# Performance work log

Hardware: AMD Instinct MI355X
Metric: run time of the kernel (lower is better)

Reference implementation:

```python
import jax, jax.numpy as jnp
import numpy as np

V, E, H = 32000, 512, 1024
S_LEN, T_LEN = 2048, 2048


def setup_inputs() -> dict:
    key = jax.random.key(0)
    ks = jax.random.split(key, 16)
    u = lambda k, shape: jax.random.uniform(k, shape, jnp.float32, -0.1, 0.1)
    return {
        "source": jax.random.randint(ks[0], (1, S_LEN), 0, V),
        "target": jax.random.randint(ks[1], (1, T_LEN), 0, V),
        "emb": u(ks[2], (V, E)),
        "enc_Wih": u(ks[3], (H, E)),
        "enc_bih": u(ks[4], (H,)),
        "enc_Whh": u(ks[5], (H, H)),
        "enc_bhh": u(ks[6], (H,)),
        "dec_Wih": u(ks[7], (H, E)),
        "dec_bih": u(ks[8], (H,)),
        "dec_Whh": u(ks[9], (H, H)),
        "dec_bhh": u(ks[10], (H,)),
        "proj_W": u(ks[11], (H, 2 * H)),
        "proj_b": u(ks[12], (H,)),
        "out_W": u(ks[13], (V, H)),
        "out_b": u(ks[14], (V,)),
    }


def _run_rnn(Wih, bih, Whh, bhh, x, h0):
    # x: [B, T, E]; vanilla RNN: h_t = tanh(x_t Wih^T + bih + h_{t-1} Whh^T + bhh)
    def step(h, xt):
        hn = jnp.tanh(xt @ Wih.T + bih + h @ Whh.T + bhh)
        return hn, hn
    h_last, ys = jax.lax.scan(step, h0, jnp.swapaxes(x, 0, 1))  # ys: [T, B, H]
    return jnp.swapaxes(ys, 0, 1), h_last


def reference(source, target, emb, enc_Wih, enc_bih, enc_Whh, enc_bhh,
              dec_Wih, dec_bih, dec_Whh, dec_bhh, proj_W, proj_b, out_W, out_b):
    B = source.shape[0]
    h0 = jnp.zeros((B, H), dtype=emb.dtype)

    src_emb = emb[source]                                        # [B, S, E]
    enc_out, h = _run_rnn(enc_Wih, enc_bih, enc_Whh, enc_bhh, src_emb, h0)
    tgt_emb = emb[target]                                        # [B, T, E]
    dec_out, _ = _run_rnn(dec_Wih, dec_bih, dec_Whh, dec_bhh, tgt_emb, h)

    # attention: target queries over source encodings
    aff = jnp.einsum('bth,bsh->bts', dec_out, enc_out)           # [B, T, S]
    attn = jax.nn.softmax(aff, axis=-1)
    ctx = jnp.einsum('bts,bsh->bth', attn, enc_out)              # [B, T, H]

    proj = jnp.concatenate([dec_out, ctx], axis=-1) @ proj_W.T + proj_b  # [B, T, H]
    scores = proj @ out_W.T + out_b                              # [B, T, V]

    logits = scores[:, :-1].reshape(-1, V)                       # [B*(T-1), V]
    tgt = target[:, 1:].reshape(-1)
    logp = jax.nn.log_softmax(logits, axis=-1)
    loss = -jnp.sum(jnp.take_along_axis(logp, tgt[:, None], axis=1))
    return loss
```

## Files before the change

### kernel.cpp

```cpp
#include <hip/hip_runtime.h>
#include <math.h>

typedef unsigned short u16;
typedef unsigned int   u32;

#define V_SZ   32000
#define E_SZ   512
#define H_SZ   1024
#define S_LEN  2048
#define T_LEN  2048
#define G_RNN  64
#define RPW    16
#define NTILE_V (V_SZ / 128)

typedef __attribute__((ext_vector_type(8))) short bf16x8;
typedef __attribute__((ext_vector_type(4))) float f32x4;
typedef __attribute__((ext_vector_type(4))) unsigned int u32x4;

typedef __attribute__((address_space(3))) void* lds_vp;
typedef const __attribute__((address_space(1))) void* gbl_vp;

__device__ __forceinline__ float bf2f(u16 u) { return __uint_as_float(((u32)u) << 16); }
__device__ __forceinline__ u16 f2bf(float f) {
  u32 x = __float_as_uint(f);
  return (u16)((x + 0x7fffu + ((x >> 16) & 1u)) >> 16);
}
__device__ __forceinline__ bool f32_bad(float f) {
  return (__float_as_uint(f) & 0x7F800000u) == 0x7F800000u;
}
__device__ __forceinline__ bool bf_bad(u16 u) { return (u & 0x7F80u) == 0x7F80u; }

__device__ __forceinline__ bf16x8 cvt8(float4 a, float4 b) {
  bf16x8 r;
  r[0] = (short)f2bf(a.x); r[1] = (short)f2bf(a.y);
  r[2] = (short)f2bf(a.z); r[3] = (short)f2bf(a.w);
  r[4] = (short)f2bf(b.x); r[5] = (short)f2bf(b.y);
  r[6] = (short)f2bf(b.z); r[7] = (short)f2bf(b.w);
  return r;
}

__global__ void sentinel_kernel(float* out) { out[0] = -400.0f; }
__global__ void diag_kernel(float* out, float code) { out[0] = code; }

__global__ __launch_bounds__(256) void init_kernel(
    const float* __restrict__ enc_bih, const float* __restrict__ enc_bhh,
    const float* __restrict__ dec_bih, const float* __restrict__ dec_bhh,
    float* biasE, float* biasD,
    u32* hsync, float* loss_acc, float* prog)
{
  int i = blockIdx.x * blockDim.x + threadIdx.x;
  if (i < H_SZ) {
    biasE[i] = enc_bih[i] + enc_bhh[i];
    biasD[i] = dec_bih[i] + dec_bhh[i];
  }
  if (i < 2 * H_SZ)
    __hip_atomic_store(hsync + i, 0u, __ATOMIC_RELAXED, __HIP_MEMORY_SCOPE_AGENT);
  if (i == 0)    { loss_acc[0] = 0.f; prog[0] = 1.0f; }
  if (i >= 1 && i < 16) prog[i] = 0.f;
}

__global__ __launch_bounds__(256) void gather_kernel(
    const float* __restrict__ emb, const int* __restrict__ ids, u16* __restrict__ dst,
    float* prog, int pidx)
{
  const int row = blockIdx.x;
  const int id  = ids[row];
  const float2* s = (const float2*)(emb + (size_t)id * E_SZ);
  const float2 v = s[threadIdx.x];
  const u32 pack = (u32)f2bf(v.x) | ((u32)f2bf(v.y) << 16);
  ((u32*)(dst + (size_t)row * E_SZ))[threadIdx.x] = pack;
  if (row == 0 && threadIdx.x == 0) prog[pidx] = 1.0f;
}

template<int MODE, int BF32>
__global__ __launch_bounds__(256) void gemm_bt(
    const u16* __restrict__ A, int lda,
    const void* __restrict__ Bp, int ldb,
    const float* __restrict__ bias,
    u16* __restrict__ Cbf, int ldc,
    float* __restrict__ stats, int ntiles, int K,
    float* prog, int pidx)
{
  __shared__ __align__(16) u16 As[128 * 32];
  __shared__ __align__(16) u16 Bs[128 * 32];
  __shared__ float sst[2][128][2];

  const int tid  = threadIdx.x;
  const int wave = tid >> 6;
  const int lane = tid & 63;
  const int quad = lane >> 4;
  const int l16  = lane & 15;
  const int m0 = blockIdx.y * 128;
  const int n0 = blockIdx.x * 128;
  const int wm = (wave >> 1) * 64;
  const int wn = (wave & 1) * 64;

  f32x4 acc[4][4];
#pragma unroll
  for (int i = 0; i < 4; ++i)
#pragma unroll
    for (int j = 0; j < 4; ++j) acc[i][j] = (f32x4){0.f, 0.f, 0.f, 0.f};

  const int srow = lane >> 2;
  const int scol = (lane & 3) * 8;
  const int c0   = wave * 2;
  const u16* ga0 = A + (size_t)(m0 + (c0 + 0) * 16 + srow) * lda + scol;
  const u16* ga1 = A + (size_t)(m0 + (c0 + 1) * 16 + srow) * lda + scol;
  const u16*   B16 = (const u16*)Bp;
  const float* B32 = (const float*)Bp;
  const u16* gb0 = B16 + (size_t)(n0 + (c0 + 0) * 16 + srow) * ldb + scol;
  const u16* gb1 = B16 + (size_t)(n0 + (c0 + 1) * 16 + srow) * ldb + scol;
  const float* fb0 = B32 + (size_t)(n0 + (c0 + 0) * 16 + srow) * ldb + scol;
  const float* fb1 = B32 + (size_t)(n0 + (c0 + 1) * 16 + srow) * ldb + scol;

  for (int k0 = 0; k0 < K; k0 += 32) {
    __builtin_amdgcn_global_load_lds((gbl_vp)(ga0 + k0), (lds_vp)(&As[(c0 + 0) * 512]), 16, 0, 0);
    __builtin_amdgcn_global_load_lds((gbl_vp)(ga1 + k0), (lds_vp)(&As[(c0 + 1) * 512]), 16, 0, 0);
    if (BF32) {
      const float* p0 = fb0 + k0;
      const float* p1 = fb1 + k0;
      const float4 a0 = *(const float4*)p0, a1 = *(const float4*)(p0 + 4);
      const float4 b0 = *(const float4*)p1, b1 = *(const float4*)(p1 + 4);
      *(bf16x8*)&Bs[(c0 + 0) * 512 + lane * 8] = cvt8(a0, a1);
      *(bf16x8*)&Bs[(c0 + 1) * 512 + lane * 8] = cvt8(b0, b1);
    } else {
      __builtin_amdgcn_global_load_lds((gbl_vp)(gb0 + k0), (lds_vp)(&Bs[(c0 + 0) * 512]), 16, 0, 0);
      __builtin_amdgcn_global_load_lds((gbl_vp)(gb1 + k0), (lds_vp)(&Bs[(c0 + 1) * 512]), 16, 0, 0);
    }
    __syncthreads();

    bf16x8 af[4], bg[4];
#pragma unroll
    for (int i = 0; i < 4; ++i) {
      af[i] = *(const bf16x8*)&As[(wm + i * 16 + l16) * 32 + quad * 8];
      bg[i] = *(const bf16x8*)&Bs[(wn + i * 16 + l16) * 32 + quad * 8];
    }
#pragma unroll
    for (int mi = 0; mi < 4; ++mi)
#pragma unroll
      for (int ni = 0; ni < 4; ++ni)
        acc[mi][ni] = __builtin_amdgcn_mfma_f32_16x16x32_bf16(af[mi], bg[ni], acc[mi][ni], 0, 0, 0);
    __syncthreads();
  }

  if (MODE == 2) {
#pragma unroll
    for (int mi = 0; mi < 4; ++mi) {
#pragma unroll
      for (int rr = 0; rr < 4; ++rr) {
        float v[4];
        float vmax = -1e30f;
#pragma unroll
        for (int ni = 0; ni < 4; ++ni) {
          const int col = n0 + wn + ni * 16 + l16;
          v[ni] = acc[mi][ni][rr] + (bias ? bias[col] : 0.f);
          vmax = fmaxf(vmax, v[ni]);
        }
        for (int d = 1; d < 16; d <<= 1) vmax = fmaxf(vmax, __shfl_xor(vmax, d, 64));
        float vs = 0.f;
#pragma unroll
        for (int ni = 0; ni < 4; ++ni) vs += expf(v[ni] - vmax);
        for (int d = 1; d < 16; d <<= 1) vs += __shfl_xor(vs, d, 64);
        if (l16 == 0) {
          const int lr = wm + mi * 16 + quad * 4 + rr;
          sst[wave & 1][lr][0] = vmax;
          sst[wave & 1][lr][1] = vs;
        }
      }
    }
    __syncthreads();
    if (tid < 128) {
      const float ma = sst[0][tid][0], sa = sst[0][tid][1];
      const float mb = sst[1][tid][0], sb = sst[1][tid][1];
      const float M = fmaxf(ma, mb);
      const float S = sa * expf(ma - M) + sb * expf(mb - M);
      const size_t row = (size_t)(m0 + tid);
      stats[(row * ntiles + blockIdx.x) * 2 + 0] = M;
      stats[(row * ntiles + blockIdx.x) * 2 + 1] = S;
    }
  } else {
#pragma unroll
    for (int mi = 0; mi < 4; ++mi)
#pragma unroll
      for (int ni = 0; ni < 4; ++ni) {
        const int col = n0 + wn + ni * 16 + l16;
        const float bb = bias ? bias[col] : 0.f;
#pragma unroll
        for (int rr = 0; rr < 4; ++rr) {
          const int row = m0 + wm + mi * 16 + quad * 4 + rr;
          Cbf[(size_t)row * ldc + col] = f2bf(acc[mi][ni][rr] + bb);
        }
      }
  }
  if (prog && blockIdx.x == 0 && blockIdx.y == 0 && tid == 0) prog[pidx] = 1.0f;
}

__global__ __launch_bounds__(256) void rnn_kernel(
    const float* __restrict__ Whh, const u16* __restrict__ pre,
    u16* __restrict__ hist, int ldh, const u16* __restrict__ h0,
    u16* __restrict__ outT,
    u32* __restrict__ hsync, int tagbase, int T, float* prog, int pidx)
{
  __shared__ float part[2][4][RPW];

  const int tid  = threadIdx.x;
  const int wg   = blockIdx.x;
  const int wv   = tid >> 6;
  const int lane = tid & 63;
  const int pr4  = tid << 2;

  float wreg[RPW][4];
#pragma unroll
  for (int r = 0; r < RPW; ++r) {
    const float4 v = *(const float4*)(Whh + (size_t)(wg * RPW + r) * H_SZ + pr4);
    wreg[r][0] = v.x; wreg[r][1] = v.y; wreg[r][2] = v.z; wreg[r][3] = v.w;
  }

  for (int t = 0; t < T; ++t) {
    float pv = 0.f;
    if (tid < RPW) pv = bf2f(pre[(size_t)t * H_SZ + wg * RPW + tid]);

    float h0v, h1v, h2v, h3v;
    if (t == 0) {
      if (h0) {
        const ushort4 hv = *(const ushort4*)(h0 + pr4);
        h0v = bf2f(hv.x); h1v = bf2f(hv.y); h2v = bf2f(hv.z); h3v = bf2f(hv.w);
      } else { h0v = h1v = h2v = h3v = 0.f; }
    } else {
      const u32 want = (u32)(tagbase + t);
      const u32* hs = hsync + (((t - 1) & 1) << 10) + pr4;
      u32 w0, w1, w2, w3;
      u32 spin = 0;
      for (;;) {
        if ((spin++ & 15u) == 15u) {
          w0 = __hip_atomic_load(hs + 0, __ATOMIC_RELAXED, __HIP_MEMORY_SCOPE_AGENT);
          w1 = __hip_atomic_load(hs + 1, __ATOMIC_RELAXED, __HIP_MEMORY_SCOPE_AGENT);
          w2 = __hip_atomic_load(hs + 2, __ATOMIC_RELAXED, __HIP_MEMORY_SCOPE_AGENT);
          w3 = __hip_atomic_load(hs + 3, __ATOMIC_RELAXED, __HIP_MEMORY_SCOPE_AGENT);
        } else {
          u32x4 x;
          asm volatile("global_load_dwordx4 %0, %1, off sc0 sc1\n\t"
                       "s_waitcnt vmcnt(0)"
                       : "=v"(x) : "v"(hs) : "memory");
          w0 = x[0]; w1 = x[1]; w2 = x[2]; w3 = x[3];
        }
        if ((w0 >> 16) == want && (w1 >> 16) == want &&
            (w2 >> 16) == want && (w3 >> 16) == want) break;
      }
      h0v = bf2f((u16)w0); h1v = bf2f((u16)w1);
      h2v = bf2f((u16)w2); h3v = bf2f((u16)w3);
    }

    float p[RPW];
#pragma unroll
    for (int r = 0; r < RPW; ++r)
      p[r] = wreg[r][0] * h0v + wreg[r][1] * h1v
           + wreg[r][2] * h2v + wreg[r][3] * h3v;

#pragma unroll
    for (int i = 0; i < 8; ++i) {
      const float send = (lane & 32) ? p[i] : p[i + 8];
      const float recv = __shfl_xor(send, 32, 64);
      const float keep = (lane & 32) ? p[i + 8] : p[i];
      p[i] = keep + recv;
    }
#pragma unroll
    for (int i = 0; i < 4; ++i) {
      const float send = (lane & 16) ? p[i] : p[i + 4];
      const float recv = __shfl_xor(send, 16, 64);
      const float keep = (lane & 16) ? p[i + 4] : p[i];
      p[i] = keep + recv;
    }
#pragma unroll
    for (int i = 0; i < 2; ++i) {
      const float send = (lane & 8) ? p[i] : p[i + 2];
      const float recv = __shfl_xor(send, 8, 64);
      const float keep = (lane & 8) ? p[i + 2] : p[i];
      p[i] = keep + recv;
    }
    {
      const float send = (lane & 4) ? p[0] : p[1];
      const float recv = __shfl_xor(send, 4, 64);
      const float keep = (lane & 4) ? p[1] : p[0];
      p[0] = keep + recv;
    }
    p[0] += __shfl_xor(p[0], 1, 64);
    p[0] += __shfl_xor(p[0], 2, 64);

    const int rown = (lane >> 2) & 15;
    if ((lane & 3) == 0) part[t & 1][wv][rown] = p[0];
    __syncthreads();

    if (tid < RPW) {
      const float s = part[t & 1][0][tid] + part[t & 1][1][tid]
                    + part[t & 1][2][tid] + part[t & 1][3][tid];
      const float hn = tanhf(pv + s);
      const u16 hv16 = f2bf(hn);
      const int gr = wg * RPW + tid;
      const u32 word = ((u32)(tagbase + t + 1) << 16) | (u32)hv16;
      __hip_atomic_store(hsync + ((t & 1) << 10) + gr, word,
                         __ATOMIC_RELAXED, __HIP_MEMORY_SCOPE_AGENT);
      hist[(size_t)t * ldh + gr] = hv16;
      if (outT) outT[(size_t)gr * S_LEN + t] = hv16;
    }
  }
  if (wg == 0 && tid == 0) prog[pidx] = 1.0f;
}

__global__ __launch_bounds__(256) void softmax_kernel(
    u16* __restrict__ aff, float* prog, int pidx)
{
  const int row = blockIdx.x;
  const int tid = threadIdx.x;
  u16* a = aff + (size_t)row * S_LEN;
  __shared__ float red[256];

  float m = -1e30f;
  for (int j = tid; j < S_LEN; j += 256) m = fmaxf(m, bf2f(a[j]));
  red[tid] = m; __syncthreads();
  for (int s = 128; s > 0; s >>= 1) { if (tid < s) red[tid] = fmaxf(red[tid], red[tid + s]); __syncthreads(); }
  const float M = red[0];
  __syncthreads();

  float sum = 0.f;
  for (int j = tid; j < S_LEN; j += 256) sum += expf(bf2f(a[j]) - M);
  red[tid] = sum; __syncthreads();
  for (int s = 128; s > 0; s >>= 1) { if (tid < s) red[tid] += red[tid + s]; __syncthreads(); }
  const float inv = 1.f / red[0];

  for (int j = tid; j < S_LEN; j += 256) {
    const float e = expf(bf2f(a[j]) - M) * inv;
    a[j] = f2bf(e);
  }
  if (row == 0 && tid == 0) prog[pidx] = 1.0f;
}

__global__ __launch_bounds__(256) void loss_kernel(
    const u16* __restrict__ proj_bf, const float* __restrict__ outW,
    const float* __restrict__ outb, const int* __restrict__ target,
    const float* __restrict__ stats, int ntiles, float* loss_acc,
    float* prog, int pidx)
{
  const int t   = blockIdx.x;
  const int tid = threadIdx.x;
  const int c   = target[t + 1];
  __shared__ float s1[256], s2[256];

  float p = 0.f;
  const u16*   pr = proj_bf + (size_t)t * H_SZ;
  const float* wr = outW + (size_t)c * H_SZ;
  for (int j = tid; j < H_SZ; j += 256) p += bf2f(pr[j]) * f2bf(wr[j]) * 0.f + bf2f(pr[j]) * bf2f(f2bf(wr[j]));
  s1[tid] = p; __syncthreads();
  for (int s = 128; s > 0; s >>= 1) { if (tid < s) s1[tid] += s1[tid + s]; __syncthreads(); }
  const float dotv = s1[0] + outb[c];

  const float* st = stats + (size_t)t * ntiles * 2;
  float mi = -1e30f, si = 0.f;
  if (tid < ntiles) { mi = st[tid * 2]; si = st[tid * 2 + 1]; }
  s2[tid] = mi; __syncthreads();
  for (int s = 128; s > 0; s >>= 1) { if (tid < s) s2[tid] = fmaxf(s2[tid], s2[tid + s]); __syncthreads(); }
  const float M = s2[0];
  const float e = (tid < ntiles) ? si * expf(mi - M) : 0.f;
  __syncthreads();
  s1[tid] = e; __syncthreads();
  for (int s = 128; s > 0; s >>= 1) { if (tid < s) s1[tid] += s1[tid + s]; __syncthreads(); }

  if (tid == 0) {
    atomicAdd(loss_acc, (M + logf(s1[0])) - dotv);
    if (t == 0) prog[pidx] = 1.0f;
  }
}

__global__ void finalize_kernel(
    const float* loss_acc, const float* prog,
    const float* biasE, const float* biasD,
    const u16* enc_out, const u16* cat, const u16* proj_bf, const float* stats,
    float* out)
{
  for (int i = 0; i < 13; ++i)
    if (prog[i] != 1.0f) { out[0] = -(100.0f + i); return; }

  const float loss = loss_acc[0];
  if (!f32_bad(loss)) { out[0] = loss; return; }

  int s = -1;
  for (int i = 0; i < 37 && s < 0; ++i)
    if (f32_bad(biasE[(i * 97) % H_SZ]) || f32_bad(biasD[(i * 97) % H_SZ])) s = 0;
  for (int i = 0; i < 37 && s < 0; ++i)
    if (bf_bad(enc_out[((size_t)i * 131071u) % (2048u * 1024u)])) s = 2;
  for (int i = 0; i < 37 && s < 0; ++i)
    if (bf_bad(cat[(((size_t)(i * 557) % 2048) * 2048) + (i * 97) % 1024])) s = 3;
  for (int i = 0; i < 37 && s < 0; ++i)
    if (bf_bad(cat[(((size_t)(i * 557) % 2048) * 2048) + 1024 + (i * 97) % 1024])) s = 5;
  for (int i = 0; i < 37 && s < 0; ++i)
    if (bf_bad(proj_bf[((size_t)i * 131071u) % (2048u * 1024u)])) s = 6;
  for (int i = 0; i < 37 && s < 0; ++i)
    if (f32_bad(stats[((size_t)i * 99991u) % (2048u * 500u)])) s = 7;
  out[0] = (s < 0) ? -300.0f : -(200.0f + 10.0f * s);
}

extern "C" void kernel_launch(void* const* d_in, const int* in_sizes, int n_in,
                              void* d_out, int out_size, void* d_ws, size_t ws_size,
                              hipStream_t stream)
{
  (void)in_sizes; (void)n_in; (void)out_size;

  const int*   src     = (const int*)d_in[0];
  const int*   tgt     = (const int*)d_in[1];
  const float* emb     = (const float*)d_in[2];
  const float* enc_Wih = (const float*)d_in[3];
  const float* enc_bih = (const float*)d_in[4];
  const float* enc_Whh = (const float*)d_in[5];
  const float* enc_bhh = (const float*)d_in[6];
  const float* dec_Wih = (const float*)d_in[7];
  const float* dec_bih = (const float*)d_in[8];
  const float* dec_Whh = (const float*)d_in[9];
  const float* dec_bhh = (const float*)d_in[10];
  const float* proj_W  = (const float*)d_in[11];
  const float* proj_b  = (const float*)d_in[12];
  const float* out_W   = (const float*)d_in[13];
  const float* out_b   = (const float*)d_in[14];

  char* wsb = (char*)d_ws;
  const size_t MB = (size_t)1 << 20;
  u16*   src_emb  = (u16*)(wsb + 0);
  u16*   tgt_emb  = (u16*)(wsb + 2 * MB);
  u16*   enc_outT = (u16*)(wsb + 0);
  u16*   proj_bf  = (u16*)(wsb + 0);
  u16*   enc_pre  = (u16*)(wsb + 4 * MB);
  u16*   dec_pre  = (u16*)(wsb + 8 * MB);
  u16*   aff      = (u16*)(wsb + 4 * MB);
  float* stats    = (float*)(wsb + 4 * MB);
  u16*   enc_out  = (u16*)(wsb + 12 * MB);
  u16*   cat      = (u16*)(wsb + 16 * MB);
  char*  tail     = wsb + 24 * MB;
  float* biasE    = (float*)tail;
  float* biasD    = biasE + H_SZ;
  float* loss_acc = biasD + H_SZ;
  float* prog     = loss_acc + 64;
  u32*   hsync    = (u32*)(prog + 64);
  const size_t need = 24 * MB + 64 * 1024;

  if (ws_size < need) {
    diag_kernel<<<1, 1, 0, stream>>>((float*)d_out, -(1000.0f + (float)(ws_size / MB)));
    return;
  }

  sentinel_kernel<<<1, 1, 0, stream>>>((float*)d_out);

  init_kernel<<<S_LEN / 256, 256, 0, stream>>>(enc_bih, enc_bhh, dec_bih, dec_bhh,
      biasE, biasD, hsync, loss_acc, prog);

  gather_kernel<<<S_LEN, 256, 0, stream>>>(emb, src, src_emb, prog, 1);
  gather_kernel<<<T_LEN, 256, 0, stream>>>(emb, tgt, tgt_emb, prog, 2);

  gemm_bt<1, 1><<<dim3(H_SZ / 128, S_LEN / 128), 256, 0, stream>>>(
      src_emb, E_SZ, enc_Wih, E_SZ, biasE, enc_pre, H_SZ, nullptr, 0, E_SZ, prog, 3);
  gemm_bt<1, 1><<<dim3(H_SZ / 128, T_LEN / 128), 256, 0, stream>>>(
      tgt_emb, E_SZ, dec_Wih, E_SZ, biasD, dec_pre, H_SZ, nullptr, 0, E_SZ, prog, 4);

  rnn_kernel<<<G_RNN, 256, 0, stream>>>(enc_Whh, enc_pre, enc_out, H_SZ, nullptr,
      enc_outT, hsync, 0, S_LEN, prog, 5);
  rnn_kernel<<<G_RNN, 256, 0, stream>>>(dec_Whh, dec_pre, cat, 2 * H_SZ,
      enc_out + (size_t)(S_LEN - 1) * H_SZ, nullptr, hsync, S_LEN, T_LEN, prog, 6);

  gemm_bt<1, 0><<<dim3(S_LEN / 128, T_LEN / 128), 256, 0, stream>>>(
      cat, 2 * H_SZ, enc_out, H_SZ, nullptr, aff, S_LEN, nullptr, 0, H_SZ, prog, 7);
  softmax_kernel<<<T_LEN, 256, 0, stream>>>(aff, prog, 8);
  gemm_bt<1, 0><<<dim3(H_SZ / 128, T_LEN / 128), 256, 0, stream>>>(
      aff, S_LEN, enc_outT, S_LEN, nullptr, cat + H_SZ, 2 * H_SZ, nullptr, 0, S_LEN, prog, 9);
  gemm_bt<1, 1><<<dim3(H_SZ / 128, T_LEN / 128), 256, 0, stream>>>(
      cat, 2 * H_SZ, proj_W, 2 * H_SZ, proj_b, proj_bf, H_SZ, nullptr, 0, 2 * H_SZ, prog, 10);
  gemm_bt<2, 1><<<dim3(NTILE_V, T_LEN / 128), 256, 0, stream>>>(
      proj_bf, H_SZ, out_W, H_SZ, out_b, nullptr, 0, stats, NTILE_V, H_SZ, prog, 11);

  loss_kernel<<<T_LEN - 1, 256, 0, stream>>>(proj_bf, out_W, out_b, tgt, stats,
      NTILE_V, loss_acc, prog, 12);

  finalize_kernel<<<1, 1, 0, stream>>>(loss_acc, prog, biasE, biasD,
      enc_out, cat, proj_bf, stats, (float*)d_out);
}
```

Before: 7.476 ms.

## Give each wavefront its own rows in RNN step to drop block barrier

Each wavefront now owns four rows of Whh and loads all 1024 columns of h (16 per lane), so the row reductions finish inside the wave with shuffles. This removes the LDS partial-sum buffer and the per-step __syncthreads, so each wave publishes its rows to the global sync array on its own. The cost is that every wave spins on and reads the whole hidden vector (four dwordx4 loads per lane instead of one per thread), which adds polling traffic, and the kernel needs more registers per thread.

Result: slower. 8.747 ms (+17.0%).

```diff
diff --git a/kernel.cpp b/kernel.cpp
--- a/kernel.cpp
+++ b/kernel.cpp
@@ -201,107 +201,120 @@
     u16* __restrict__ outT,
     u32* __restrict__ hsync, int tagbase, int T, float* prog, int pidx)
 {
-  __shared__ float part[2][4][RPW];
-
-  const int tid  = threadIdx.x;
-  const int wg   = blockIdx.x;
-  const int wv   = tid >> 6;
-  const int lane = tid & 63;
-  const int pr4  = tid << 2;
-
-  float wreg[RPW][4];
-#pragma unroll
-  for (int r = 0; r < RPW; ++r) {
-    const float4 v = *(const float4*)(Whh + (size_t)(wg * RPW + r) * H_SZ + pr4);
-    wreg[r][0] = v.x; wreg[r][1] = v.y; wreg[r][2] = v.z; wreg[r][3] = v.w;
+  const int tid   = threadIdx.x;
+  const int wg    = blockIdx.x;
+  const int wv    = tid >> 6;
+  const int lane  = tid & 63;
+  const int kb    = lane << 4;
+  const int myrow = wg * RPW + wv * 4 + (lane >> 4);
+  const bool pubL = (lane & 15) == 0;
+
+  float wreg[4][16];
+#pragma unroll
+  for (int r = 0; r < 4; ++r) {
+    const float* wrow = Whh + (size_t)(wg * RPW + wv * 4 + r) * H_SZ + kb;
+#pragma unroll
+    for (int j = 0; j < 4; ++j) {
+      const float4 v = *(const float4*)(wrow + j * 4);
+      wreg[r][j * 4 + 0] = v.x; wreg[r][j * 4 + 1] = v.y;
+      wreg[r][j * 4 + 2] = v.z; wreg[r][j * 4 + 3] = v.w;
+    }
   }
 
   for (int t = 0; t < T; ++t) {
     float pv = 0.f;
-    if (tid < RPW) pv = bf2f(pre[(size_t)t * H_SZ + wg * RPW + tid]);
-
-    float h0v, h1v, h2v, h3v;
+    if (pubL) pv = bf2f(pre[(size_t)t * H_SZ + myrow]);
+
+    float hv[16];
     if (t == 0) {
       if (h0) {
-        const ushort4 hv = *(const ushort4*)(h0 + pr4);
-        h0v = bf2f(hv.x); h1v = bf2f(hv.y); h2v = bf2f(hv.z); h3v = bf2f(hv.w);
-      } else { h0v = h1v = h2v = h3v = 0.f; }
+#pragma unroll
+        for (int j = 0; j < 4; ++j) {
+          const ushort4 u = *(const ushort4*)(h0 + kb + j * 4);
+          hv[j * 4 + 0] = bf2f(u.x); hv[j * 4 + 1] = bf2f(u.y);
+          hv[j * 4 + 2] = bf2f(u.z); hv[j * 4 + 3] = bf2f(u.w);
+        }
+      } else {
+#pragma unroll
+        for (int j = 0; j < 16; ++j) hv[j] = 0.f;
+      }
     } else {
       const u32 want = (u32)(tagbase + t);
-      const u32* hs = hsync + (((t - 1) & 1) << 10) + pr4;
-      u32 w0, w1, w2, w3;
+      const u32* hs = hsync + (((t - 1) & 1) << 10) + kb;
+      u32x4 x0, x1, x2, x3;
       u32 spin = 0;
       for (;;) {
         if ((spin++ & 15u) == 15u) {
-          w0 = __hip_atomic_load(hs + 0, __ATOMIC_RELAXED, __HIP_MEMORY_SCOPE_AGENT);
-          w1 = __hip_atomic_load(hs + 1, __ATOMIC_RELAXED, __HIP_MEMORY_SCOPE_AGENT);
-          w2 = __hip_atomic_load(hs + 2, __ATOMIC_RELAXED, __HIP_MEMORY_SCOPE_AGENT);
-          w3 = __hip_atomic_load(hs + 3, __ATOMIC_RELAXED, __HIP_MEMORY_SCOPE_AGENT);
+#pragma unroll
+          for (int j = 0; j < 4; ++j) {
+            x0[j] = __hip_atomic_load(hs + j,      __ATOMIC_RELAXED, __HIP_MEMORY_SCOPE_AGENT);
+            x1[j] = __hip_atomic_load(hs + 4 + j,  __ATOMIC_RELAXED, __HIP_MEMORY_SCOPE_AGENT);
+            x2[j] = __hip_atomic_load(hs + 8 + j,  __ATOMIC_RELAXED, __HIP_MEMORY_SCOPE_AGENT);
+            x3[j] = __hip_atomic_load(hs + 12 + j, __ATOMIC_RELAXED, __HIP_MEMORY_SCOPE_AGENT);
+          }
         } else {
-          u32x4 x;
-          asm volatile("global_load_dwordx4 %0, %1, off sc0 sc1\n\t"
-                       "s_waitcnt vmcnt(0)"
-                       : "=v"(x) : "v"(hs) : "memory");
-          w0 = x[0]; w1 = x[1]; w2 = x[2]; w3 = x[3];
-        }
-        if ((w0 >> 16) == want && (w1 >> 16) == want &&
-            (w2 >> 16) == want && (w3 >> 16) == want) break;
+          asm volatile(
+              "global_load_dwordx4 %0, %4, off sc0 sc1\n\t"
+              "global_load_dwordx4 %1, %4, off offset:16 sc0 sc1\n\t"
+              "global_load_dwordx4 %2, %4, off offset:32 sc0 sc1\n\t"
+              "global_load_dwordx4 %3, %4, off offset:48 sc0 sc1\n\t"
+              "s_waitcnt vmcnt(0)"
+              : "=&v"(x0), "=&v"(x1), "=&v"(x2), "=&v"(x3)
+              : "v"(hs) : "memory");
+        }
+        bool ok = true;
+#pragma unroll
+        for (int j = 0; j < 4; ++j) {
+          ok = ok && ((x0[j] >> 16) == want) && ((x1[j] >> 16) == want)
+                  && ((x2[j] >> 16) == want) && ((x3[j] >> 16) == want);
+        }
+        if (ok) break;
       }
-      h0v = bf2f((u16)w0); h1v = bf2f((u16)w1);
-      h2v = bf2f((u16)w2); h3v = bf2f((u16)w3);
-    }
-
-    float p[RPW];
-#pragma unroll
-    for (int r = 0; r < RPW; ++r)
-      p[r] = wreg[r][0] * h0v + wreg[r][1] * h1v
-           + wreg[r][2] * h2v + wreg[r][3] * h3v;
-
-#pragma unroll
-    for (int i = 0; i < 8; ++i) {
-      const float send = (lane & 32) ? p[i] : p[i + 8];
+#pragma unroll
+      for (int j = 0; j < 4; ++j) {
+        hv[j]      = bf2f((u16)x0[j]);
+        hv[4 + j]  = bf2f((u16)x1[j]);
+        hv[8 + j]  = bf2f((u16)x2[j]);
+        hv[12 + j] = bf2f((u16)x3[j]);
+      }
+    }
+
+    float p[4] = {0.f, 0.f, 0.f, 0.f};
+#pragma unroll
+    for (int j = 0; j < 16; ++j) {
+      const float h = hv[j];
+      p[0] += wreg[0][j] * h;
+      p[1] += wreg[1][j] * h;
+      p[2] += wreg[2][j] * h;
+      p[3] += wreg[3][j] * h;
+    }
+
+#pragma unroll
+    for (int i = 0; i < 2; ++i) {
+      const float send = (lane & 32) ? p[i] : p[i + 2];
       const float recv = __shfl_xor(send, 32, 64);
-      const float keep = (lane & 32) ? p[i + 8] : p[i];
+      const float keep = (lane & 32) ? p[i + 2] : p[i];
       p[i] = keep + recv;
     }
-#pragma unroll
-    for (int i = 0; i < 4; ++i) {
-      const float send = (lane & 16) ? p[i] : p[i + 4];
+    {
+      const float send = (lane & 16) ? p[0] : p[1];
       const float recv = __shfl_xor(send, 16, 64);
-      const float keep = (lane & 16) ? p[i + 4] : p[i];
-      p[i] = keep + recv;
-    }
-#pragma unroll
-    for (int i = 0; i < 2; ++i) {
-      const float send = (lane & 8) ? p[i] : p[i + 2];
-      const float recv = __shfl_xor(send, 8, 64);
-      const float keep = (lane & 8) ? p[i + 2] : p[i];
-      p[i] = keep + recv;
-    }
-    {
-      const float send = (lane & 4) ? p[0] : p[1];
-      const float recv = __shfl_xor(send, 4, 64);
-      const float keep = (lane & 4) ? p[1] : p[0];
+      const float keep = (lane & 16) ? p[1] : p[0];
       p[0] = keep + recv;
     }
+    p[0] += __shfl_xor(p[0], 8, 64);
+    p[0] += __shfl_xor(p[0], 4, 64);
+    p[0] += __shfl_xor(p[0], 2, 64);
     p[0] += __shfl_xor(p[0], 1, 64);
-    p[0] += __shfl_xor(p[0], 2, 64);
-
-    const int rown = (lane >> 2) & 15;
-    if ((lane & 3) == 0) part[t & 1][wv][rown] = p[0];
-    __syncthreads();
-
-    if (tid < RPW) {
-      const float s = part[t & 1][0][tid] + part[t & 1][1][tid]
-                    + part[t & 1][2][tid] + part[t & 1][3][tid];
-      const float hn = tanhf(pv + s);
+
+    if (pubL) {
+      const float hn = tanhf(pv + p[0]);
       const u16 hv16 = f2bf(hn);
-      const int gr = wg * RPW + tid;
       const u32 word = ((u32)(tagbase + t + 1) << 16) | (u32)hv16;
-      __hip_atomic_store(hsync + ((t & 1) << 10) + gr, word,
+      __hip_atomic_store(hsync + ((t & 1) << 10) + myrow, word,
                          __ATOMIC_RELAXED, __HIP_MEMORY_SCOPE_AGENT);
-      hist[(size_t)t * ldh + gr] = hv16;
-      if (outT) outT[(size_t)gr * S_LEN + t] = hv16;
+      hist[(size_t)t * ldh + myrow] = hv16;
+      if (outT) outT[(size_t)myrow * S_LEN + t] = hv16;
     }
   }
   if (wg == 0 && tid == 0) prog[pidx] = 1.0f;
```
